# Kernel optimization log

Hardware: AMD Instinct MI355X
Metric: run time of the kernel (lower is better)

Reference implementation:

```python
import jax, jax.numpy as jnp
import numpy as np


def setup_inputs() -> dict:
    key = jax.random.key(0)
    k1, k2 = jax.random.split(key)
    B, C, H, W = 16, 256, 64, 64
    K, D = 1024, 256
    z = jax.random.normal(k1, (B, C, H, W), dtype=jnp.float32)
    embedding = jax.random.normal(k2, (K, D), dtype=jnp.float32)
    return {"z": z, "embedding": embedding}


def reference(z, embedding):
    # _preprocess: shift channel dim (axis 1) to last, flatten -> [N, D]
    B, C, H, W = z.shape
    encoded_permuted = jnp.transpose(z, (0, 2, 3, 1))  # [B, H, W, C]
    permuted_shape = encoded_permuted.shape
    encoded_flat = encoded_permuted.reshape(-1, C)  # [N, D]

    x_sq = jnp.sum(encoded_flat * encoded_flat, axis=1, keepdims=True)  # [N, 1]
    e_sq = jnp.sum(embedding * embedding, axis=1)  # [K]
    cross = encoded_flat @ embedding.T  # [N, K]
    distances = x_sq - 2.0 * cross + e_sq[None, :]
    codebook_indices = jnp.argmin(distances, axis=1)  # [N]
    quantized_lookup = embedding[codebook_indices]  # [N, D]

    # straight-through estimator
    quantized_flat = encoded_flat + jax.lax.stop_gradient(quantized_lookup - encoded_flat)

    # _postprocess: reshape and shift last dim back to axis 1
    quantized = jnp.transpose(quantized_flat.reshape(permuted_shape), (0, 3, 1, 2))
    return (encoded_flat, quantized_flat, codebook_indices, quantized)
```

## Files before the change

kernel.cpp:

```cpp
#include <hip/hip_runtime.h>
#include <hip/hip_bf16.h>

typedef _Float16 h8 __attribute__((ext_vector_type(8)));
typedef float f4 __attribute__((ext_vector_type(4)));

#define N_TOK 65536
#define DIM 256
#define KCODES 1024
#define HWSZ 4096

__device__ __forceinline__ void gll16(const void* g, void* l) {
    __builtin_amdgcn_global_load_lds((const __attribute__((address_space(1))) void*)g,
                                     (__attribute__((address_space(3))) void*)l, 16, 0, 0);
}


__global__ void k_prep_frag(const float* __restrict__ emb, _Float16* __restrict__ BhF,
                            _Float16* __restrict__ BlF) {
    int gi = blockIdx.x * 256 + threadIdx.x;
    int kb = gi >> 9;
    int s = (gi >> 6) & 7;
    int dq = (gi >> 4) & 3;
    int r = gi & 15;
    int code = kb * 16 + r;
    int d0 = s * 32 + dq * 8;
    const float* src = emb + (size_t)code * DIM + d0;
    float4 x0 = *(const float4*)(src);
    float4 x1 = *(const float4*)(src + 4);
    float xs[8] = {x0.x, x0.y, x0.z, x0.w, x1.x, x1.y, x1.z, x1.w};
    h8 hi, lo;
#pragma unroll
    for (int j = 0; j < 8; ++j) {
        _Float16 h = (_Float16)xs[j];
        hi[j] = h;
        lo[j] = (_Float16)(xs[j] - (float)h);
    }
    *(h8*)(BhF + (size_t)gi * 8) = hi;
    *(h8*)(BlF + (size_t)gi * 8) = lo;
}

__global__ void k_esq(const float* __restrict__ emb, float* __restrict__ e_sq) {
    int t = threadIdx.x;
    int code = blockIdx.x * 4 + (t >> 6);
    int l = t & 63;
    float4 v = *(const float4*)(emb + (size_t)code * DIM + l * 4);
    float s = v.x * v.x + v.y * v.y + v.z * v.z + v.w * v.w;
#pragma unroll
    for (int off = 32; off >= 1; off >>= 1) s += __shfl_xor(s, off);
    if (l == 0) e_sq[code] = s;
}

__global__ void k_transpose(const float* __restrict__ z, float* __restrict__ enc,
                            _Float16* __restrict__ AhF, _Float16* __restrict__ AlF) {
    __shared__ float T[64][65];
    int blk = blockIdx.x;
    int b = blk >> 8;
    int rem = blk & 255;
    int c0 = (rem >> 6) * 64;
    int hw0 = (rem & 63) * 64;
    int t = threadIdx.x;
    const float* zp = z + (size_t)b * DIM * HWSZ;
    {
        int hw4 = (t & 15) * 4, cl = t >> 4;
#pragma unroll
        for (int i = 0; i < 4; ++i) {
            int c = cl + i * 16;
            float4 v = *(const float4*)(zp + (size_t)(c0 + c) * HWSZ + hw0 + hw4);
            T[c][hw4 + 0] = v.x; T[c][hw4 + 1] = v.y;
            T[c][hw4 + 2] = v.z; T[c][hw4 + 3] = v.w;
        }
    }
    __syncthreads();
    {
        int c4 = (t & 15) * 4, hwl = t >> 4;
#pragma unroll
        for (int i = 0; i < 4; ++i) {
            int hw = hwl + i * 16;
            float4 v;
            v.x = T[c4 + 0][hw]; v.y = T[c4 + 1][hw];
            v.z = T[c4 + 2][hw]; v.w = T[c4 + 3][hw];
            *(float4*)(enc + (size_t)(b * HWSZ + hw0 + hw) * DIM + c0 + c4) = v;
        }
    }
    {
        int base_nb = b * 256 + (hw0 >> 4);
#pragma unroll
        for (int i = 0; i < 2; ++i) {
            int gidx = i * 256 + t;
            int nbi = gidx >> 7;
            int si = (gidx >> 6) & 1;
            int dq = (gidx >> 4) & 3;
            int r = gidx & 15;
            int hwl = nbi * 16 + r;
            int cl = si * 32 + dq * 8;
            h8 hi, lo;
#pragma unroll
            for (int j = 0; j < 8; ++j) {
                float x = T[cl + j][hwl];
                _Float16 h = (_Float16)x;
                hi[j] = h;
                lo[j] = (_Float16)(x - (float)h);
            }
            size_t G = (((size_t)(base_nb + nbi) * 8) + (c0 >> 5) + si) * 64 + dq * 16 + r;
            *(h8*)(AhF + G * 8) = hi;
            *(h8*)(AlF + G * 8) = lo;
        }
    }
}

__global__ __launch_bounds__(512)
void k_gemm_argmin(const _Float16* __restrict__ AhF, const _Float16* __restrict__ AlF,
                   const _Float16* __restrict__ BhF, const _Float16* __restrict__ BlF,
                   const float* __restrict__ e_sq,
                   float* __restrict__ partV, int* __restrict__ partI) {
    __shared__ _Float16 sAh[4096];
    __shared__ _Float16 sAl[4096];
    __shared__ _Float16 sBh[8192];
    __shared__ _Float16 sBl[8192];

    int gid = blockIdx.x;
    int colTile = gid >> 9, rowTile = gid & 511;
    int r0 = rowTile * 128, c0 = colTile * 256;
    int t = threadIdx.x;
    int w = t >> 6, l = t & 63;
    int wm = w >> 2, wn = w & 3;
    int l16 = l & 15, lhi = l >> 4;

    const char* gAh = (const char*)AhF + (((size_t)(rowTile * 8 + w)) << 13) + (l << 4);
    const char* gAl = (const char*)AlF + (((size_t)(rowTile * 8 + w)) << 13) + (l << 4);
    const char* gBh0 = (const char*)BhF + (((size_t)(colTile * 16 + w)) << 13) + (l << 4);
    const char* gBh1 = gBh0 + (8ll << 13);
    const char* gBl0 = (const char*)BlF + (((size_t)(colTile * 16 + w)) << 13) + (l << 4);
    const char* gBl1 = gBl0 + (8ll << 13);
    char* lAh = (char*)sAh + (w << 10);
    char* lAl = (char*)sAl + (w << 10);
    char* lBh0 = (char*)sBh + (w << 10);
    char* lBh1 = (char*)sBh + ((8 + w) << 10);
    char* lBl0 = (char*)sBl + (w << 10);
    char* lBl1 = (char*)sBl + ((8 + w) << 10);

    f4 acc[4][4];
#pragma unroll
    for (int i = 0; i < 4; ++i)
#pragma unroll
        for (int j = 0; j < 4; ++j) acc[i][j] = (f4)0.0f;

    for (int s = 0; s < 8; ++s) {
        size_t so = (size_t)s << 10;
        gll16(gAh + so, lAh);
        gll16(gAl + so, lAl);
        gll16(gBh0 + so, lBh0);
        gll16(gBh1 + so, lBh1);
        gll16(gBl0 + so, lBl0);
        gll16(gBl1 + so, lBl1);
        __syncthreads();

        h8 ah[4], al[4], bh[4], bl[4];
#pragma unroll
        for (int mf = 0; mf < 4; ++mf) {
            ah[mf] = *(const h8*)(sAh + (((wm * 4 + mf) << 9) + (l << 3)));
            al[mf] = *(const h8*)(sAl + (((wm * 4 + mf) << 9) + (l << 3)));
        }
#pragma unroll
        for (int nf = 0; nf < 4; ++nf) {
            bh[nf] = *(const h8*)(sBh + (((wn * 4 + nf) << 9) + (l << 3)));
            bl[nf] = *(const h8*)(sBl + (((wn * 4 + nf) << 9) + (l << 3)));
        }
#pragma unroll
        for (int mf = 0; mf < 4; ++mf)
#pragma unroll
            for (int nf = 0; nf < 4; ++nf) {
                acc[mf][nf] = __builtin_amdgcn_mfma_f32_16x16x32_f16(ah[mf], bh[nf], acc[mf][nf], 0, 0, 0);
                acc[mf][nf] = __builtin_amdgcn_mfma_f32_16x16x32_f16(ah[mf], bl[nf], acc[mf][nf], 0, 0, 0);
                acc[mf][nf] = __builtin_amdgcn_mfma_f32_16x16x32_f16(al[mf], bh[nf], acc[mf][nf], 0, 0, 0);
            }
        __syncthreads();
    }

    float* sminV = (float*)sAh;
    int* sminI = (int*)sAl;

    float esq[4];
#pragma unroll
    for (int nf = 0; nf < 4; ++nf) esq[nf] = e_sq[c0 + wn * 64 + nf * 16 + l16];

#pragma unroll
    for (int mf = 0; mf < 4; ++mf) {
#pragma unroll
        for (int rg = 0; rg < 4; ++rg) {
            float bestV = 3.4e38f;
            int bestI = 0;
#pragma unroll
            for (int nf = 0; nf < 4; ++nf) {
                float v = esq[nf] - 2.0f * acc[mf][nf][rg];
                int ci = c0 + wn * 64 + nf * 16 + l16;
                if (v < bestV || (v == bestV && ci < bestI)) { bestV = v; bestI = ci; }
            }
#pragma unroll
            for (int off = 1; off < 16; off <<= 1) {
                float vv = __shfl_xor(bestV, off);
                int ii = __shfl_xor(bestI, off);
                if (vv < bestV || (vv == bestV && ii < bestI)) { bestV = vv; bestI = ii; }
            }
            if (l16 == 0) {
                int rloc = wm * 64 + mf * 16 + lhi * 4 + rg;
                sminV[wn * 128 + rloc] = bestV;
                sminI[wn * 128 + rloc] = bestI;
            }
        }
    }
    __syncthreads();
    if (t < 128) {
        float bestV = sminV[t];
        int bestI = sminI[t];
#pragma unroll
        for (int wn2 = 1; wn2 < 4; ++wn2) {
            float v = sminV[wn2 * 128 + t];
            int i2 = sminI[wn2 * 128 + t];
            if (v < bestV || (v == bestV && i2 < bestI)) { bestV = v; bestI = i2; }
        }
        partV[colTile * N_TOK + r0 + t] = bestV;
        partI[colTile * N_TOK + r0 + t] = bestI;
    }
}

__global__ void k_final_idx(const float* __restrict__ partV, const int* __restrict__ partI,
                            float* __restrict__ out2, int* __restrict__ idxI) {
    int n = blockIdx.x * 256 + threadIdx.x;
    float bestV = partV[n];
    int bestI = partI[n];
#pragma unroll
    for (int ct = 1; ct < 4; ++ct) {
        float v = partV[ct * N_TOK + n];
        int i2 = partI[ct * N_TOK + n];
        if (v < bestV || (v == bestV && i2 < bestI)) { bestV = v; bestI = i2; }
    }
    out2[n] = (float)bestI;
    idxI[n] = bestI;
}

__global__ void k_out1(const float* __restrict__ emb, const int* __restrict__ idxI,
                       float* __restrict__ out1) {
    int t = threadIdx.x;
    int r = blockIdx.x * 64 + (t >> 2), q = t & 3;
    int idx = idxI[r];
    const float* src = emb + (size_t)idx * DIM + q * 64;
    float* dst = out1 + (size_t)r * DIM + q * 64;
#pragma unroll
    for (int i = 0; i < 16; ++i)
        *(float4*)(dst + i * 4) = *(const float4*)(src + i * 4);
}

__global__ void k_out3(const float* __restrict__ emb, const int* __restrict__ idxI,
                       float* __restrict__ out3) {
    __shared__ float E[32][257];
    int blk = blockIdx.x;
    int b = blk >> 7, hwt = blk & 127;
    int hw0 = hwt * 32;
    int n0 = b * HWSZ + hw0;
    int t = threadIdx.x;
    {
        int r = t >> 3, oct = t & 7;
        int idx = idxI[n0 + r];
        const float* src = emb + (size_t)idx * DIM + oct * 32;
#pragma unroll
        for (int i = 0; i < 8; ++i) {
            float4 v = *(const float4*)(src + i * 4);
            E[r][oct * 32 + i * 4 + 0] = v.x;
            E[r][oct * 32 + i * 4 + 1] = v.y;
            E[r][oct * 32 + i * 4 + 2] = v.z;
            E[r][oct * 32 + i * 4 + 3] = v.w;
        }
    }
    __syncthreads();
    {
        int w = t >> 6, l = t & 63;
        int ch = l >> 5, hw = l & 31;
        float* dst = out3 + (size_t)b * DIM * HWSZ + hw0 + hw;
#pragma unroll
        for (int it = 0; it < 32; ++it) {
            int c = w * 64 + it * 2 + ch;
            dst[(size_t)c * HWSZ] = E[hw][c];
        }
    }
}

extern "C" void kernel_launch(void* const* d_in, const int* in_sizes, int n_in,
                              void* d_out, int out_size, void* d_ws, size_t ws_size,
                              hipStream_t stream) {
    const float* z = (const float*)d_in[0];
    const float* emb = (const float*)d_in[1];
    float* out = (float*)d_out;
    float* out0 = out;
    float* out1 = out + 16777216;
    float* out2 = out + 33554432;
    float* out3 = out + 33619968;

    _Float16* AhF = (_Float16*)out1;
    _Float16* AlF = (_Float16*)(out1 + 8388608);

    char* ws = (char*)d_ws;
    _Float16* BhF = (_Float16*)(ws);
    _Float16* BlF = (_Float16*)(ws + 524288);
    float* e_sq = (float*)(ws + 1048576);
    float* partV = (float*)(ws + 1052672);
    int* partI = (int*)(ws + 2101248);
    int* idxI = (int*)(ws + 3149824);

    k_prep_frag<<<128, 256, 0, stream>>>(emb, BhF, BlF);
    k_esq<<<256, 256, 0, stream>>>(emb, e_sq);
    k_transpose<<<4096, 256, 0, stream>>>(z, out0, AhF, AlF);
    k_gemm_argmin<<<2048, 512, 0, stream>>>(AhF, AlF, BhF, BlF, e_sq, partV, partI);
    k_final_idx<<<256, 256, 0, stream>>>(partV, partI, out2, idxI);
    k_out1<<<1024, 256, 0, stream>>>(emb, idxI, out1);
    k_out3<<<2048, 256, 0, stream>>>(emb, idxI, out3);
}
```

Before: 237.6 us.

## Use single fp16 GEMM with margin-flagged fp32 rescoring of ambiguous rows

Drops the hi/lo split-fp16 scheme and runs one fp16 MFMA per tile instead of three. The kernel now tracks the best and second-best distance so rows whose margin is below a fixed threshold can be flagged. Flagged rows are re-scored exactly in fp32 against all codes, and the GEMM k-loop gains double-buffered LDS loads. The cost is extra argmin bookkeeping plus a rescoring kernel, and a fixed TAU and list cap (FCAP) that could miss near-ties or overflow on other data.

```diff
diff --git a/kernel.cpp b/kernel.cpp
--- a/kernel.cpp
+++ b/kernel.cpp
@@ -8,6 +8,8 @@
 #define DIM 256
 #define KCODES 1024
 #define HWSZ 4096
+#define TAU 0.125f
+#define FCAP 8192
 
 __device__ __forceinline__ void gll16(const void* g, void* l) {
     __builtin_amdgcn_global_load_lds((const __attribute__((address_space(1))) void*)g,
@@ -15,8 +17,7 @@
 }
 
 
-__global__ void k_prep_frag(const float* __restrict__ emb, _Float16* __restrict__ BhF,
-                            _Float16* __restrict__ BlF) {
+__global__ void k_prep_frag(const float* __restrict__ emb, _Float16* __restrict__ BhF) {
     int gi = blockIdx.x * 256 + threadIdx.x;
     int kb = gi >> 9;
     int s = (gi >> 6) & 7;
@@ -28,18 +29,15 @@
     float4 x0 = *(const float4*)(src);
     float4 x1 = *(const float4*)(src + 4);
     float xs[8] = {x0.x, x0.y, x0.z, x0.w, x1.x, x1.y, x1.z, x1.w};
-    h8 hi, lo;
-#pragma unroll
-    for (int j = 0; j < 8; ++j) {
-        _Float16 h = (_Float16)xs[j];
-        hi[j] = h;
-        lo[j] = (_Float16)(xs[j] - (float)h);
-    }
+    h8 hi;
+#pragma unroll
+    for (int j = 0; j < 8; ++j) hi[j] = (_Float16)xs[j];
     *(h8*)(BhF + (size_t)gi * 8) = hi;
-    *(h8*)(BlF + (size_t)gi * 8) = lo;
-}
-
-__global__ void k_esq(const float* __restrict__ emb, float* __restrict__ e_sq) {
+}
+
+__global__ void k_esq(const float* __restrict__ emb, float* __restrict__ e_sq,
+                      int* __restrict__ flagCnt) {
+    if (blockIdx.x == 0 && threadIdx.x == 0) *flagCnt = 0;
     int t = threadIdx.x;
     int code = blockIdx.x * 4 + (t >> 6);
     int l = t & 63;
@@ -51,7 +49,7 @@
 }
 
 __global__ void k_transpose(const float* __restrict__ z, float* __restrict__ enc,
-                            _Float16* __restrict__ AhF, _Float16* __restrict__ AlF) {
+                            _Float16* __restrict__ AhF) {
     __shared__ float T[64][65];
     int blk = blockIdx.x;
     int b = blk >> 8;
@@ -93,30 +91,21 @@
             int r = gidx & 15;
             int hwl = nbi * 16 + r;
             int cl = si * 32 + dq * 8;
-            h8 hi, lo;
-#pragma unroll
-            for (int j = 0; j < 8; ++j) {
-                float x = T[cl + j][hwl];
-                _Float16 h = (_Float16)x;
-                hi[j] = h;
-                lo[j] = (_Float16)(x - (float)h);
-            }
+            h8 hi;
+#pragma unroll
+            for (int j = 0; j < 8; ++j) hi[j] = (_Float16)T[cl + j][hwl];
             size_t G = (((size_t)(base_nb + nbi) * 8) + (c0 >> 5) + si) * 64 + dq * 16 + r;
             *(h8*)(AhF + G * 8) = hi;
-            *(h8*)(AlF + G * 8) = lo;
         }
     }
 }
 
 __global__ __launch_bounds__(512)
-void k_gemm_argmin(const _Float16* __restrict__ AhF, const _Float16* __restrict__ AlF,
-                   const _Float16* __restrict__ BhF, const _Float16* __restrict__ BlF,
+void k_gemm_argmin(const _Float16* __restrict__ AhF, const _Float16* __restrict__ BhF,
                    const float* __restrict__ e_sq,
-                   float* __restrict__ partV, int* __restrict__ partI) {
-    __shared__ _Float16 sAh[4096];
-    __shared__ _Float16 sAl[4096];
-    __shared__ _Float16 sBh[8192];
-    __shared__ _Float16 sBl[8192];
+                   float* __restrict__ pV1, int* __restrict__ pI1,
+                   float* __restrict__ pV2) {
+    __shared__ _Float16 S[2][12288];
 
     int gid = blockIdx.x;
     int colTile = gid >> 9, rowTile = gid & 511;
@@ -126,18 +115,12 @@
     int wm = w >> 2, wn = w & 3;
     int l16 = l & 15, lhi = l >> 4;
 
-    const char* gAh = (const char*)AhF + (((size_t)(rowTile * 8 + w)) << 13) + (l << 4);
-    const char* gAl = (const char*)AlF + (((size_t)(rowTile * 8 + w)) << 13) + (l << 4);
-    const char* gBh0 = (const char*)BhF + (((size_t)(colTile * 16 + w)) << 13) + (l << 4);
-    const char* gBh1 = gBh0 + (8ll << 13);
-    const char* gBl0 = (const char*)BlF + (((size_t)(colTile * 16 + w)) << 13) + (l << 4);
-    const char* gBl1 = gBl0 + (8ll << 13);
-    char* lAh = (char*)sAh + (w << 10);
-    char* lAl = (char*)sAl + (w << 10);
-    char* lBh0 = (char*)sBh + (w << 10);
-    char* lBh1 = (char*)sBh + ((8 + w) << 10);
-    char* lBl0 = (char*)sBl + (w << 10);
-    char* lBl1 = (char*)sBl + ((8 + w) << 10);
+    const char* gA = (const char*)AhF + (((size_t)(rowTile * 8 + w)) << 13) + (l << 4);
+    const char* gB0 = (const char*)BhF + (((size_t)(colTile * 16 + w)) << 13) + (l << 4);
+    const char* gB1 = gB0 + (8ll << 13);
+    int aoff = w << 10;
+    int boff0 = 8192 + (w << 10);
+    int boff1 = 8192 + ((8 + w) << 10);
 
     f4 acc[4][4];
 #pragma unroll
@@ -145,40 +128,37 @@
 #pragma unroll
         for (int j = 0; j < 4; ++j) acc[i][j] = (f4)0.0f;
 
+    gll16(gA, (char*)S[0] + aoff);
+    gll16(gB0, (char*)S[0] + boff0);
+    gll16(gB1, (char*)S[0] + boff1);
+    __syncthreads();
+
     for (int s = 0; s < 8; ++s) {
-        size_t so = (size_t)s << 10;
-        gll16(gAh + so, lAh);
-        gll16(gAl + so, lAl);
-        gll16(gBh0 + so, lBh0);
-        gll16(gBh1 + so, lBh1);
-        gll16(gBl0 + so, lBl0);
-        gll16(gBl1 + so, lBl1);
+        int cur = s & 1;
+        if (s < 7) {
+            size_t so = (size_t)(s + 1) << 10;
+            gll16(gA + so, (char*)S[cur ^ 1] + aoff);
+            gll16(gB0 + so, (char*)S[cur ^ 1] + boff0);
+            gll16(gB1 + so, (char*)S[cur ^ 1] + boff1);
+        }
+        h8 ah[4], bh[4];
+#pragma unroll
+        for (int mf = 0; mf < 4; ++mf)
+            ah[mf] = *(const h8*)((const char*)S[cur] + (((wm * 4 + mf) << 10) + (l << 4)));
+#pragma unroll
+        for (int nf = 0; nf < 4; ++nf)
+            bh[nf] = *(const h8*)((const char*)S[cur] + 8192 + (((wn * 4 + nf) << 10) + (l << 4)));
+#pragma unroll
+        for (int mf = 0; mf < 4; ++mf)
+#pragma unroll
+            for (int nf = 0; nf < 4; ++nf)
+                acc[mf][nf] = __builtin_amdgcn_mfma_f32_16x16x32_f16(ah[mf], bh[nf], acc[mf][nf], 0, 0, 0);
         __syncthreads();
-
-        h8 ah[4], al[4], bh[4], bl[4];
-#pragma unroll
-        for (int mf = 0; mf < 4; ++mf) {
-            ah[mf] = *(const h8*)(sAh + (((wm * 4 + mf) << 9) + (l << 3)));
-            al[mf] = *(const h8*)(sAl + (((wm * 4 + mf) << 9) + (l << 3)));
-        }
-#pragma unroll
-        for (int nf = 0; nf < 4; ++nf) {
-            bh[nf] = *(const h8*)(sBh + (((wn * 4 + nf) << 9) + (l << 3)));
-            bl[nf] = *(const h8*)(sBl + (((wn * 4 + nf) << 9) + (l << 3)));
-        }
-#pragma unroll
-        for (int mf = 0; mf < 4; ++mf)
-#pragma unroll
-            for (int nf = 0; nf < 4; ++nf) {
-                acc[mf][nf] = __builtin_amdgcn_mfma_f32_16x16x32_f16(ah[mf], bh[nf], acc[mf][nf], 0, 0, 0);
-                acc[mf][nf] = __builtin_amdgcn_mfma_f32_16x16x32_f16(ah[mf], bl[nf], acc[mf][nf], 0, 0, 0);
-                acc[mf][nf] = __builtin_amdgcn_mfma_f32_16x16x32_f16(al[mf], bh[nf], acc[mf][nf], 0, 0, 0);
-            }
-        __syncthreads();
-    }
-
-    float* sminV = (float*)sAh;
-    int* sminI = (int*)sAl;
+    }
+
+    float* smV1 = (float*)S[0];
+    int* smI1 = (int*)S[0] + 512;
+    float* smV2 = (float*)S[0] + 1024;
 
     float esq[4];
 #pragma unroll
@@ -188,55 +168,108 @@
     for (int mf = 0; mf < 4; ++mf) {
 #pragma unroll
         for (int rg = 0; rg < 4; ++rg) {
-            float bestV = 3.4e38f;
-            int bestI = 0;
+            float v1 = 3.4e38f, v2 = 3.4e38f;
+            int i1 = 0;
 #pragma unroll
             for (int nf = 0; nf < 4; ++nf) {
                 float v = esq[nf] - 2.0f * acc[mf][nf][rg];
                 int ci = c0 + wn * 64 + nf * 16 + l16;
-                if (v < bestV || (v == bestV && ci < bestI)) { bestV = v; bestI = ci; }
+                if (v < v1 || (v == v1 && ci < i1)) { v2 = v1; v1 = v; i1 = ci; }
+                else v2 = fminf(v2, v);
             }
 #pragma unroll
             for (int off = 1; off < 16; off <<= 1) {
-                float vv = __shfl_xor(bestV, off);
-                int ii = __shfl_xor(bestI, off);
-                if (vv < bestV || (vv == bestV && ii < bestI)) { bestV = vv; bestI = ii; }
+                float ov1 = __shfl_xor(v1, off);
+                int oi1 = __shfl_xor(i1, off);
+                float ov2 = __shfl_xor(v2, off);
+                if (ov1 < v1 || (ov1 == v1 && oi1 < i1)) { v2 = fminf(v1, ov2); v1 = ov1; i1 = oi1; }
+                else v2 = fminf(v2, ov1);
             }
             if (l16 == 0) {
                 int rloc = wm * 64 + mf * 16 + lhi * 4 + rg;
-                sminV[wn * 128 + rloc] = bestV;
-                sminI[wn * 128 + rloc] = bestI;
+                smV1[wn * 128 + rloc] = v1;
+                smI1[wn * 128 + rloc] = i1;
+                smV2[wn * 128 + rloc] = v2;
             }
         }
     }
     __syncthreads();
     if (t < 128) {
-        float bestV = sminV[t];
-        int bestI = sminI[t];
+        float v1 = smV1[t], v2 = smV2[t];
+        int i1 = smI1[t];
 #pragma unroll
         for (int wn2 = 1; wn2 < 4; ++wn2) {
-            float v = sminV[wn2 * 128 + t];
-            int i2 = sminI[wn2 * 128 + t];
-            if (v < bestV || (v == bestV && i2 < bestI)) { bestV = v; bestI = i2; }
-        }
-        partV[colTile * N_TOK + r0 + t] = bestV;
-        partI[colTile * N_TOK + r0 + t] = bestI;
-    }
-}
-
-__global__ void k_final_idx(const float* __restrict__ partV, const int* __restrict__ partI,
-                            float* __restrict__ out2, int* __restrict__ idxI) {
+            float a1 = smV1[wn2 * 128 + t];
+            int ai = smI1[wn2 * 128 + t];
+            float a2 = smV2[wn2 * 128 + t];
+            if (a1 < v1 || (a1 == v1 && ai < i1)) { v2 = fminf(v1, a2); v1 = a1; i1 = ai; }
+            else v2 = fminf(v2, a1);
+        }
+        pV1[colTile * N_TOK + r0 + t] = v1;
+        pI1[colTile * N_TOK + r0 + t] = i1;
+        pV2[colTile * N_TOK + r0 + t] = v2;
+    }
+}
+
+__global__ void k_final_idx(const float* __restrict__ pV1, const int* __restrict__ pI1,
+                            const float* __restrict__ pV2,
+                            float* __restrict__ out2, int* __restrict__ idxI,
+                            int* __restrict__ flagCnt, int* __restrict__ flagList) {
     int n = blockIdx.x * 256 + threadIdx.x;
-    float bestV = partV[n];
-    int bestI = partI[n];
+    float v1 = pV1[n], v2 = pV2[n];
+    int i1 = pI1[n];
 #pragma unroll
     for (int ct = 1; ct < 4; ++ct) {
-        float v = partV[ct * N_TOK + n];
-        int i2 = partI[ct * N_TOK + n];
-        if (v < bestV || (v == bestV && i2 < bestI)) { bestV = v; bestI = i2; }
-    }
-    out2[n] = (float)bestI;
-    idxI[n] = bestI;
+        float a1 = pV1[ct * N_TOK + n];
+        int ai = pI1[ct * N_TOK + n];
+        float a2 = pV2[ct * N_TOK + n];
+        if (a1 < v1 || (a1 == v1 && ai < i1)) { v2 = fminf(v1, a2); v1 = a1; i1 = ai; }
+        else v2 = fminf(v2, a1);
+    }
+    out2[n] = (float)i1;
+    idxI[n] = i1;
+    if (v2 - v1 < TAU) {
+        int p = atomicAdd(flagCnt, 1);
+        if (p < FCAP) flagList[p] = n;
+    }
+}
+
+__global__ __launch_bounds__(512)
+void k_rescore(const float* __restrict__ enc, const float* __restrict__ emb,
+               const int* __restrict__ flagCnt, const int* __restrict__ flagList,
+               float* __restrict__ out2, int* __restrict__ idxI) {
+    __shared__ float sv[8];
+    __shared__ int si[8];
+    int cnt = *flagCnt;
+    if (cnt > FCAP) cnt = FCAP;
+    int t = threadIdx.x, w = t >> 6, l = t & 63;
+    for (int j = blockIdx.x; j < cnt; j += gridDim.x) {
+        int row = flagList[j];
+        f4 x = *(const f4*)(enc + (size_t)row * DIM + l * 4);
+        float bv = 3.4e38f;
+        int bi = 0;
+        for (int c = w; c < KCODES; c += 8) {
+            f4 e = *(const f4*)(emb + (size_t)c * DIM + l * 4);
+            float p = e[0] * (e[0] - 2.0f * x[0]) + e[1] * (e[1] - 2.0f * x[1]) +
+                      e[2] * (e[2] - 2.0f * x[2]) + e[3] * (e[3] - 2.0f * x[3]);
+#pragma unroll
+            for (int off = 32; off >= 1; off >>= 1) p += __shfl_xor(p, off);
+            if (p < bv) { bv = p; bi = c; }
+        }
+        if (l == 0) { sv[w] = bv; si[w] = bi; }
+        __syncthreads();
+        if (t == 0) {
+            float fv = sv[0];
+            int fi = si[0];
+#pragma unroll
+            for (int k = 1; k < 8; ++k) {
+                if (sv[k] < fv || (sv[k] == fv && si[k] < fi)) { fv = sv[k]; fi = si[k]; }
+            }
+            out2[row] = (float)fi;
+            idxI[row] = fi;
+        }
+        __syncthreads();
+    }
 }
 
 __global__ void k_out1(const float* __restrict__ emb, const int* __restrict__ idxI,
@@ -297,21 +330,23 @@
     float* out3 = out + 33619968;
 
     _Float16* AhF = (_Float16*)out1;
-    _Float16* AlF = (_Float16*)(out1 + 8388608);
+    float* pV1 = out1 + 8388608;
+    int* pI1 = (int*)(out1 + 8650752);
+    float* pV2 = out1 + 8912896;
 
     char* ws = (char*)d_ws;
     _Float16* BhF = (_Float16*)(ws);
-    _Float16* BlF = (_Float16*)(ws + 524288);
-    float* e_sq = (float*)(ws + 1048576);
-    float* partV = (float*)(ws + 1052672);
-    int* partI = (int*)(ws + 2101248);
-    int* idxI = (int*)(ws + 3149824);
-
-    k_prep_frag<<<128, 256, 0, stream>>>(emb, BhF, BlF);
-    k_esq<<<256, 256, 0, stream>>>(emb, e_sq);
-    k_transpose<<<4096, 256, 0, stream>>>(z, out0, AhF, AlF);
-    k_gemm_argmin<<<2048, 512, 0, stream>>>(AhF, AlF, BhF, BlF, e_sq, partV, partI);
-    k_final_idx<<<256, 256, 0, stream>>>(partV, partI, out2, idxI);
+    float* e_sq = (float*)(ws + 524288);
+    int* flagCnt = (int*)(ws + 528384);
+    int* flagList = (int*)(ws + 532480);
+    int* idxI = (int*)(ws + 565248);
+
+    k_prep_frag<<<128, 256, 0, stream>>>(emb, BhF);
+    k_esq<<<256, 256, 0, stream>>>(emb, e_sq, flagCnt);
+    k_transpose<<<4096, 256, 0, stream>>>(z, out0, AhF);
+    k_gemm_argmin<<<2048, 512, 0, stream>>>(AhF, BhF, e_sq, pV1, pI1, pV2);
+    k_final_idx<<<256, 256, 0, stream>>>(pV1, pI1, pV2, out2, idxI, flagCnt, flagList);
+    k_rescore<<<512, 512, 0, stream>>>(out0, emb, flagCnt, flagList, out2, idxI);
     k_out1<<<1024, 256, 0, stream>>>(emb, idxI, out1);
     k_out3<<<2048, 256, 0, stream>>>(emb, idxI, out3);
 }
```

Measured after the change: 311.6 us. 1.31x slower.

## Load GEMM fragments directly from global memory into registers, drop LDS staging

Applied to the files above, without the earlier changes.

The GEMM-argmin kernel no longer stages A/B hi/lo fragments through shared memory with global_load_lds and barriers. Each wave now loads its own fragments straight from global memory into registers and reorders the three MFMA passes so the lo loads can overlap the earlier MFMAs. This removes two block barriers per K step and the LDS round trip. In exchange, data shared between waves is fetched redundantly from global/L2, about four times more global traffic per block. Renaming the partial buffers has no speed effect.

```diff
diff --git a/kernel.cpp b/kernel.cpp
--- a/kernel.cpp
+++ b/kernel.cpp
@@ -8,11 +8,6 @@
 #define DIM 256
 #define KCODES 1024
 #define HWSZ 4096
-
-__device__ __forceinline__ void gll16(const void* g, void* l) {
-    __builtin_amdgcn_global_load_lds((const __attribute__((address_space(1))) void*)g,
-                                     (__attribute__((address_space(3))) void*)l, 16, 0, 0);
-}
 
 
 __global__ void k_prep_frag(const float* __restrict__ emb, _Float16* __restrict__ BhF,
@@ -112,11 +107,9 @@
 void k_gemm_argmin(const _Float16* __restrict__ AhF, const _Float16* __restrict__ AlF,
                    const _Float16* __restrict__ BhF, const _Float16* __restrict__ BlF,
                    const float* __restrict__ e_sq,
-                   float* __restrict__ partV, int* __restrict__ partI) {
-    __shared__ _Float16 sAh[4096];
-    __shared__ _Float16 sAl[4096];
-    __shared__ _Float16 sBh[8192];
-    __shared__ _Float16 sBl[8192];
+                   float* __restrict__ pV1, int* __restrict__ pI1) {
+    __shared__ float smV[512];
+    __shared__ int smI[512];
 
     int gid = blockIdx.x;
     int colTile = gid >> 9, rowTile = gid & 511;
@@ -126,18 +119,10 @@
     int wm = w >> 2, wn = w & 3;
     int l16 = l & 15, lhi = l >> 4;
 
-    const char* gAh = (const char*)AhF + (((size_t)(rowTile * 8 + w)) << 13) + (l << 4);
-    const char* gAl = (const char*)AlF + (((size_t)(rowTile * 8 + w)) << 13) + (l << 4);
-    const char* gBh0 = (const char*)BhF + (((size_t)(colTile * 16 + w)) << 13) + (l << 4);
-    const char* gBh1 = gBh0 + (8ll << 13);
-    const char* gBl0 = (const char*)BlF + (((size_t)(colTile * 16 + w)) << 13) + (l << 4);
-    const char* gBl1 = gBl0 + (8ll << 13);
-    char* lAh = (char*)sAh + (w << 10);
-    char* lAl = (char*)sAl + (w << 10);
-    char* lBh0 = (char*)sBh + (w << 10);
-    char* lBh1 = (char*)sBh + ((8 + w) << 10);
-    char* lBl0 = (char*)sBl + (w << 10);
-    char* lBl1 = (char*)sBl + ((8 + w) << 10);
+    const char* pAh = (const char*)AhF + (((size_t)(rowTile * 8 + wm * 4)) << 13) + (l << 4);
+    const char* pAl = (const char*)AlF + (((size_t)(rowTile * 8 + wm * 4)) << 13) + (l << 4);
+    const char* pBh = (const char*)BhF + (((size_t)(colTile * 16 + wn * 4)) << 13) + (l << 4);
+    const char* pBl = (const char*)BlF + (((size_t)(colTile * 16 + wn * 4)) << 13) + (l << 4);
 
     f4 acc[4][4];
 #pragma unroll
@@ -145,40 +130,36 @@
 #pragma unroll
         for (int j = 0; j < 4; ++j) acc[i][j] = (f4)0.0f;
 
+#pragma unroll 2
     for (int s = 0; s < 8; ++s) {
-        size_t so = (size_t)s << 10;
-        gll16(gAh + so, lAh);
-        gll16(gAl + so, lAl);
-        gll16(gBh0 + so, lBh0);
-        gll16(gBh1 + so, lBh1);
-        gll16(gBl0 + so, lBl0);
-        gll16(gBl1 + so, lBl1);
-        __syncthreads();
-
-        h8 ah[4], al[4], bh[4], bl[4];
-#pragma unroll
-        for (int mf = 0; mf < 4; ++mf) {
-            ah[mf] = *(const h8*)(sAh + (((wm * 4 + mf) << 9) + (l << 3)));
-            al[mf] = *(const h8*)(sAl + (((wm * 4 + mf) << 9) + (l << 3)));
-        }
-#pragma unroll
-        for (int nf = 0; nf < 4; ++nf) {
-            bh[nf] = *(const h8*)(sBh + (((wn * 4 + nf) << 9) + (l << 3)));
-            bl[nf] = *(const h8*)(sBl + (((wn * 4 + nf) << 9) + (l << 3)));
-        }
+        int off = s << 10;
+        h8 ah[4], bh[4];
+#pragma unroll
+        for (int mf = 0; mf < 4; ++mf) ah[mf] = *(const h8*)(pAh + (mf << 13) + off);
+#pragma unroll
+        for (int nf = 0; nf < 4; ++nf) bh[nf] = *(const h8*)(pBh + (nf << 13) + off);
 #pragma unroll
         for (int mf = 0; mf < 4; ++mf)
 #pragma unroll
-            for (int nf = 0; nf < 4; ++nf) {
+            for (int nf = 0; nf < 4; ++nf)
                 acc[mf][nf] = __builtin_amdgcn_mfma_f32_16x16x32_f16(ah[mf], bh[nf], acc[mf][nf], 0, 0, 0);
+        h8 al[4];
+#pragma unroll
+        for (int mf = 0; mf < 4; ++mf) al[mf] = *(const h8*)(pAl + (mf << 13) + off);
+#pragma unroll
+        for (int mf = 0; mf < 4; ++mf)
+#pragma unroll
+            for (int nf = 0; nf < 4; ++nf)
+                acc[mf][nf] = __builtin_amdgcn_mfma_f32_16x16x32_f16(al[mf], bh[nf], acc[mf][nf], 0, 0, 0);
+        h8 bl[4];
+#pragma unroll
+        for (int nf = 0; nf < 4; ++nf) bl[nf] = *(const h8*)(pBl + (nf << 13) + off);
+#pragma unroll
+        for (int mf = 0; mf < 4; ++mf)
+#pragma unroll
+            for (int nf = 0; nf < 4; ++nf)
                 acc[mf][nf] = __builtin_amdgcn_mfma_f32_16x16x32_f16(ah[mf], bl[nf], acc[mf][nf], 0, 0, 0);
-                acc[mf][nf] = __builtin_amdgcn_mfma_f32_16x16x32_f16(al[mf], bh[nf], acc[mf][nf], 0, 0, 0);
-            }
-        __syncthreads();
-    }
-
-    float* sminV = (float*)sAh;
-    int* sminI = (int*)sAl;
+    }
 
     float esq[4];
 #pragma unroll
@@ -204,39 +185,39 @@
             }
             if (l16 == 0) {
                 int rloc = wm * 64 + mf * 16 + lhi * 4 + rg;
-                sminV[wn * 128 + rloc] = bestV;
-                sminI[wn * 128 + rloc] = bestI;
+                smV[wn * 128 + rloc] = bestV;
+                smI[wn * 128 + rloc] = bestI;
             }
         }
     }
     __syncthreads();
     if (t < 128) {
-        float bestV = sminV[t];
-        int bestI = sminI[t];
+        float bestV = smV[t];
+        int bestI = smI[t];
 #pragma unroll
         for (int wn2 = 1; wn2 < 4; ++wn2) {
-            float v = sminV[wn2 * 128 + t];
-            int i2 = sminI[wn2 * 128 + t];
+            float v = smV[wn2 * 128 + t];
+            int i2 = smI[wn2 * 128 + t];
             if (v < bestV || (v == bestV && i2 < bestI)) { bestV = v; bestI = i2; }
         }
-        partV[colTile * N_TOK + r0 + t] = bestV;
-        partI[colTile * N_TOK + r0 + t] = bestI;
-    }
-}
-
-__global__ void k_final_idx(const float* __restrict__ partV, const int* __restrict__ partI,
+        pV1[colTile * N_TOK + r0 + t] = bestV;
+        pI1[colTile * N_TOK + r0 + t] = bestI;
+    }
+}
+
+__global__ void k_final_idx(const float* __restrict__ pV1, const int* __restrict__ pI1,
                             float* __restrict__ out2, int* __restrict__ idxI) {
     int n = blockIdx.x * 256 + threadIdx.x;
-    float bestV = partV[n];
-    int bestI = partI[n];
+    float v1 = pV1[n];
+    int i1 = pI1[n];
 #pragma unroll
     for (int ct = 1; ct < 4; ++ct) {
-        float v = partV[ct * N_TOK + n];
-        int i2 = partI[ct * N_TOK + n];
-        if (v < bestV || (v == bestV && i2 < bestI)) { bestV = v; bestI = i2; }
-    }
-    out2[n] = (float)bestI;
-    idxI[n] = bestI;
+        float a1 = pV1[ct * N_TOK + n];
+        int ai = pI1[ct * N_TOK + n];
+        if (a1 < v1 || (a1 == v1 && ai < i1)) { v1 = a1; i1 = ai; }
+    }
+    out2[n] = (float)i1;
+    idxI[n] = i1;
 }
 
 __global__ void k_out1(const float* __restrict__ emb, const int* __restrict__ idxI,
@@ -303,15 +284,15 @@
     _Float16* BhF = (_Float16*)(ws);
     _Float16* BlF = (_Float16*)(ws + 524288);
     float* e_sq = (float*)(ws + 1048576);
-    float* partV = (float*)(ws + 1052672);
-    int* partI = (int*)(ws + 2101248);
+    float* pV1 = (float*)(ws + 1052672);
+    int* pI1 = (int*)(ws + 2101248);
     int* idxI = (int*)(ws + 3149824);
 
     k_prep_frag<<<128, 256, 0, stream>>>(emb, BhF, BlF);
     k_esq<<<256, 256, 0, stream>>>(emb, e_sq);
     k_transpose<<<4096, 256, 0, stream>>>(z, out0, AhF, AlF);
-    k_gemm_argmin<<<2048, 512, 0, stream>>>(AhF, AlF, BhF, BlF, e_sq, partV, partI);
-    k_final_idx<<<256, 256, 0, stream>>>(partV, partI, out2, idxI);
+    k_gemm_argmin<<<2048, 512, 0, stream>>>(AhF, AlF, BhF, BlF, e_sq, pV1, pI1);
+    k_final_idx<<<256, 256, 0, stream>>>(pV1, pI1, out2, idxI);
     k_out1<<<1024, 256, 0, stream>>>(emb, idxI, out1);
     k_out3<<<2048, 256, 0, stream>>>(emb, idxI, out3);
 }
```

After: 275.3 us. +15.9%, slower.
